# Performance work log

Measured on AMD Instinct MI355X. Metric: run time of the kernel, lower is better.

The kernel has to match this reference:

```python
import jax, jax.numpy as jnp
import numpy as np

B, S, M, K, V, E, NQ, C = 1024, 512, 64, 64, 128, 64, 10000, 4


def setup_inputs() -> dict:
    key = jax.random.key(0)
    ks = jax.random.split(key, 12)
    sc = 0.05  # small init so attention logits / predictions stay sane
    return {
        "q_ids": jax.random.randint(ks[0], (B, S), 0, NQ),
        "responses": jax.random.randint(ks[1], (B, S), 0, C),
        "q_table": jax.random.normal(ks[2], (NQ + 1, E), jnp.float32),
        "key_embeds": jax.random.normal(ks[3], (M, K), jnp.float32) * sc,
        "alpha_mean": jnp.zeros((M,), jnp.float32),
        "alpha_log_var": jnp.full((M,), np.log(0.3), jnp.float32),
        "beta_base": jnp.zeros((M,), jnp.float32),
        "beta_offsets": jnp.full((M, C - 1), 0.5, jnp.float32),
        "theta_mean0": jnp.zeros((M, V), jnp.float32),
        "theta_log_var0": jnp.zeros((M, V), jnp.float32),
        "q2k_w": jax.random.normal(ks[4], (E, K), jnp.float32) * sc,
        "q2k_b": jnp.zeros((K,), jnp.float32),
        "qa_w": jax.random.normal(ks[5], (2, E), jnp.float32) * sc,
        "qa_b": jnp.zeros((E,), jnp.float32),
        "qae_w": jax.random.normal(ks[6], (E, V), jnp.float32) * sc,
        "qae_b": jnp.zeros((V,), jnp.float32),
        "pred_w": jax.random.normal(ks[7], (V, 1), jnp.float32) * sc,
        "pred_b": jnp.zeros((1,), jnp.float32),
        "alpha_noise": jax.random.normal(ks[8], (S, M), jnp.float32),
        "beta_noise": jax.random.normal(ks[9], (S, M), jnp.float32),
    }


def reference(q_ids, responses, q_table, key_embeds, alpha_mean, alpha_log_var,
              beta_base, beta_offsets, theta_mean0, theta_log_var0,
              q2k_w, q2k_b, qa_w, qa_b, qae_w, qae_b, pred_w, pred_b,
              alpha_noise, beta_noise):
    # ---- question embeddings and DKVMN queries ----
    q_emb = q_table[q_ids]                                   # [B,S,E]
    query = q_emb @ q2k_w + q2k_b                            # [B,S,K]
    embed_sim = jnp.einsum('bsk,mk->bsm', query, key_embeds) # [B,S,M]

    # ---- per-slot IRT parameter sampling (vectorized over all 64 slots) ----
    alpha = jnp.exp(alpha_mean[None] + alpha_noise * jnp.exp(0.5 * alpha_log_var)[None])  # [S,M]
    base = beta_base[None] + beta_noise * 0.1                # [S,M]
    offs = jax.nn.softplus(beta_offsets)                     # [M,C-1]
    # beta[j] = base + sum_{k<j} offsets[k]  (ordered cumulative thresholds)
    cum = jnp.concatenate([jnp.zeros((M, 1), offs.dtype),
                           jnp.cumsum(offs, axis=1)[:, :C - 2]], axis=1)  # [M,C-1]
    beta_mean = base + cum.mean(axis=1)[None]                # [S,M]
    diff_sim = jnp.exp(-0.5 * beta_mean ** 2)                # [S,M]

    logits = embed_sim + 0.3 * alpha[None] + 0.2 * diff_sim[None]
    attn = jax.nn.softmax(logits, axis=-1)                   # [B,S,M]

    # ---- response evidence ----
    r_norm = responses.astype(jnp.float32) / (C - 1)         # [B,S]
    p = jnp.clip(r_norm, 0.01, 0.99)
    ability_ev = jnp.log(p) - jnp.log1p(-p)                  # logit, [B,S]
    ev_prec = 0.5 + jnp.abs(r_norm - 0.5) * 2.0              # [B,S]
    qa_in = jnp.stack([q_ids.astype(jnp.float32) / NQ, r_norm], axis=-1)  # [B,S,2]
    ev_embed = (qa_in @ qa_w + qa_b) @ qae_w + qae_b         # [B,S,V]

    # ---- sequential read / Bayesian write over memory state ----
    def step(carry, xs):
        th_m, th_lv = carry                                  # [M,V] each
        a, ee, ae, pr = xs                                   # [B,M],[B,V],[B],[B]
        # Bayesian read: attention-weighted belief mean
        cm = a @ th_m                                        # [B,V]
        pred = (cm @ pred_w + pred_b)[:, 0]                  # [B]
        # Bayesian write (torch does this under no_grad)
        a_norm = a / (a.sum(0) + 1e-8)                       # [B,M]
        comb = (ee + ae[:, None]) * 0.5                      # [B,V]
        agg_ev = jnp.einsum('bv,bm->mv', comb, a * a_norm)   # [M,V]
        agg_pr = a_norm.T @ pr                               # [M]
        w = a.mean(0)                                        # [M] update weight per slot
        prior_pr = jnp.exp(-th_lv)
        post_pr = prior_pr + (agg_pr * w)[:, None]
        post_m = (prior_pr * th_m + (agg_pr * w)[:, None] * agg_ev) / post_pr
        return (post_m, -jnp.log(post_pr)), pred

    xs = (attn.transpose(1, 0, 2), ev_embed.transpose(1, 0, 2),
          ability_ev.T, ev_prec.T)
    _, preds = jax.lax.scan(step, (theta_mean0, theta_log_var0), xs)
    return preds.T  # [B,S] predicted ability per (student, timestep)
```

## Files before the change

kernel.cpp:

```cpp
#include <hip/hip_runtime.h>


#define WS_EQ     0
#define WS_EB     640064
#define WS_PACK   672832
#define WS_PAT    1197120
#define WS_W1     1393728
#define WS_RDEN   1426496
#define WS_CONST  1950784
#define WS_P0     1950800
#define WS_Z0     1950864

__device__ __forceinline__ float wred_sum(float x) {
    x += __shfl_xor(x, 1);
    x += __shfl_xor(x, 2);
    x += __shfl_xor(x, 4);
    x += __shfl_xor(x, 8);
    x += __shfl_xor(x, 16);
    x += __shfl_xor(x, 32);
    return x;
}

__device__ __forceinline__ float softplusf(float x) {
    return fmaxf(x, 0.0f) + log1pf(__expf(-fabsf(x)));
}

__global__ __launch_bounds__(256) void k_prep(
    const int* __restrict__ q_ids, const int* __restrict__ responses,
    const float* __restrict__ q_table, const float* __restrict__ key_embeds,
    const float* __restrict__ q2k_w, const float* __restrict__ q2k_b,
    const float* __restrict__ alpha_mean, const float* __restrict__ alpha_log_var,
    const float* __restrict__ beta_base, const float* __restrict__ beta_offsets,
    const float* __restrict__ alpha_noise, const float* __restrict__ beta_noise,
    const float* __restrict__ qa_w, const float* __restrict__ qa_b,
    const float* __restrict__ qae_w, const float* __restrict__ qae_b,
    const float* __restrict__ pred_w,
    const float* __restrict__ th0, const float* __restrict__ lv0,
    float* __restrict__ ws)
{
    const int tid = threadIdx.x;
    const int bid = blockIdx.x;
    if (bid < 626) {
        __shared__ float sw[64 * 64];
        __shared__ float ske[64 * 65];
        for (int i = tid; i < 4096; i += 256) sw[i] = q2k_w[i];
        for (int i = tid; i < 4096; i += 256) ske[(i >> 6) * 65 + (i & 63)] = key_embeds[i];
        __syncthreads();
        const int wid = tid >> 6, lane = tid & 63;
        float* eq = ws + WS_EQ;
        for (int qq = 0; qq < 4; ++qq) {
            int q = bid * 16 + wid * 4 + qq;
            int qc = (q < 10001) ? q : 10000;
            float qe = q_table[qc * 64 + lane];
            float qk = q2k_b[lane];
            #pragma unroll
            for (int e = 0; e < 64; ++e)
                qk = fmaf(__shfl(qe, e), sw[e * 64 + lane], qk);
            float sim = 0.0f;
            #pragma unroll
            for (int k = 0; k < 64; ++k)
                sim = fmaf(__shfl(qk, k), ske[lane * 65 + k], sim);
            if (q < 10001) eq[q * 64 + lane] = __expf(sim);
        }
    } else if (bid < 658) {
        float* eb = ws + WS_EB;
        int base = (bid - 626) * 1024 + tid * 4;
        #pragma unroll
        for (int j = 0; j < 4; ++j) {
            int idx = base + j;
            int m = idx & 63;
            float sdev  = __expf(0.5f * alpha_log_var[m]);
            float alpha = __expf(fmaf(alpha_noise[idx], sdev, alpha_mean[m]));
            float bse   = fmaf(beta_noise[idx], 0.1f, beta_base[m]);
            float o0 = softplusf(beta_offsets[m * 3 + 0]);
            float o1 = softplusf(beta_offsets[m * 3 + 1]);
            float cmean = (o0 + (o0 + o1)) * (1.0f / 3.0f);
            float bm = bse + cmean;
            float diff = __expf(-0.5f * bm * bm);
            eb[idx] = __expf(fmaf(0.3f, alpha, 0.2f * diff));
        }
    } else if (bid == 658) {
        const int wid = tid >> 6, lane = tid & 63;
        if (wid == 0) {
            float qv = 0.0f;
            for (int v = 0; v < 128; ++v) qv = fmaf(qae_w[lane * 128 + v], pred_w[v], qv);
            float du  = wred_sum(qa_w[lane] * qv);
            float dw  = wred_sum(qa_w[64 + lane] * qv);
            float dc1 = wred_sum(qa_b[lane] * qv);
            float cb  = wred_sum(fmaf(qae_b[lane], pred_w[lane],
                                      qae_b[64 + lane] * pred_w[64 + lane]));
            float sp  = wred_sum(pred_w[lane] + pred_w[64 + lane]);
            if (lane == 0) {
                float* c = ws + WS_CONST;
                c[0] = du; c[1] = dw; c[2] = dc1 + cb; c[3] = sp;
            }
        } else if (wid == 1) {
            float z0 = 0.0f;
            for (int v = 0; v < 128; ++v) z0 = fmaf(th0[lane * 128 + v], pred_w[v], z0);
            ws[WS_Z0 + lane] = z0;
            ws[WS_P0 + lane] = __expf(-lv0[lane * 128]);
        }
    } else {
        int tb = bid - 659;
        int sb = tb & 7;
        int bb = tb >> 3;
        __shared__ int tile[64][65];
        #pragma unroll
        for (int j = 0; j < 16; ++j) {
            int row = (tid >> 6) * 16 + j;
            int col = tid & 63;
            int gi = (bb * 64 + row) * 512 + sb * 64 + col;
            tile[row][col] = q_ids[gi] | (responses[gi] << 16);
        }
        __syncthreads();
        int* packT = (int*)(ws + WS_PACK);
        #pragma unroll
        for (int j = 0; j < 16; ++j) {
            int row = (tid >> 6) * 16 + j;
            int col = tid & 63;
            packT[(sb * 64 + row) * 1024 + bb * 64 + col] = tile[col][row];
        }
    }
}

__global__ __launch_bounds__(512) void k_reduce(float* __restrict__ ws)
{
    const int bid = blockIdx.x;
    const int t = bid & 511, h = bid >> 9;
    const int tid = threadIdx.x;
    const int wid = tid >> 6, lane = tid & 63;
    const int r = lane >> 4, c = lane & 15;
    const float* eq = ws + WS_EQ;
    const int* packT = (const int*)(ws + WS_PACK);
    const float* cst = ws + WS_CONST;
    float* rden = ws + WS_RDEN;
    const float du = cst[0], dw = cst[1], dc = cst[2], sp = cst[3];

    float ae0, ae1, ae2, ae3;
    {
        float p;
        p = 0.01f;        ae0 = logf(p) - log1pf(-p);
        p = 0.33333334f;  ae1 = logf(p) - log1pf(-p);
        p = 0.6666667f;   ae2 = logf(p) - log1pf(-p);
        p = 0.99f;        ae3 = logf(p) - log1pf(-p);
    }

    const float4 ebv = *(const float4*)(ws + WS_EB + t * 64 + c * 4);
    const int bbase = h * 512 + wid * 64;

    float4 a1v = {0.f,0.f,0.f,0.f}, a2v = {0.f,0.f,0.f,0.f}, a3v = {0.f,0.f,0.f,0.f};
    #pragma unroll 4
    for (int i = 0; i < 16; ++i) {
        int b = bbase + i * 4 + r;
        int pk = packT[t * 1024 + b];
        int qid  = pk & 0xFFFF;
        int resp = pk >> 16;
        float rn = (float)resp * 0.33333334f;
        float ae = (resp == 0) ? ae0 : (resp == 1) ? ae1 : (resp == 2) ? ae2 : ae3;
        float pv = fmaf(fabsf(rn - 0.5f), 2.0f, 0.5f);
        float yv = fmaf(ae, sp, fmaf(rn, dw, fmaf((float)qid * 1e-4f, du, dc)));
        float4 eqv = *(const float4*)(eq + qid * 64 + c * 4);
        float4 e4;
        e4.x = eqv.x * ebv.x; e4.y = eqv.y * ebv.y;
        e4.z = eqv.z * ebv.z; e4.w = eqv.w * ebv.w;
        float s = (e4.x + e4.y) + (e4.z + e4.w);
        s += __shfl_xor(s, 1);
        s += __shfl_xor(s, 2);
        s += __shfl_xor(s, 4);
        s += __shfl_xor(s, 8);
        float rinv = __builtin_amdgcn_rcpf(s);
        if (c == 0) rden[b * 512 + t] = rinv;
        float4 a4;
        a4.x = e4.x * rinv; a4.y = e4.y * rinv; a4.z = e4.z * rinv; a4.w = e4.w * rinv;
        a1v.x += a4.x; a1v.y += a4.y; a1v.z += a4.z; a1v.w += a4.w;
        a2v.x = fmaf(a4.x, pv, a2v.x); a2v.y = fmaf(a4.y, pv, a2v.y);
        a2v.z = fmaf(a4.z, pv, a2v.z); a2v.w = fmaf(a4.w, pv, a2v.w);
        a3v.x = fmaf(a4.x * a4.x, yv, a3v.x); a3v.y = fmaf(a4.y * a4.y, yv, a3v.y);
        a3v.z = fmaf(a4.z * a4.z, yv, a3v.z); a3v.w = fmaf(a4.w * a4.w, yv, a3v.w);
    }
    #pragma unroll
    for (int d = 16; d <= 32; d <<= 1) {
        a1v.x += __shfl_xor(a1v.x, d); a1v.y += __shfl_xor(a1v.y, d);
        a1v.z += __shfl_xor(a1v.z, d); a1v.w += __shfl_xor(a1v.w, d);
        a2v.x += __shfl_xor(a2v.x, d); a2v.y += __shfl_xor(a2v.y, d);
        a2v.z += __shfl_xor(a2v.z, d); a2v.w += __shfl_xor(a2v.w, d);
        a3v.x += __shfl_xor(a3v.x, d); a3v.y += __shfl_xor(a3v.y, d);
        a3v.z += __shfl_xor(a3v.z, d); a3v.w += __shfl_xor(a3v.w, d);
    }

    __shared__ float red[8][3][64];
    if (lane < 16) {
        *(float4*)&red[wid][0][lane * 4] = a1v;
        *(float4*)&red[wid][1][lane * 4] = a2v;
        *(float4*)&red[wid][2][lane * 4] = a3v;
    }
    __syncthreads();
    if (wid == 0) {
        float A1 = 0.f, A2 = 0.f, A3 = 0.f;
        #pragma unroll
        for (int w = 0; w < 8; ++w) {
            A1 += red[w][0][lane]; A2 += red[w][1][lane]; A3 += red[w][2][lane];
        }
        float* pat = ws + WS_PAT;
        pat[(h * 64 + lane) * 512 + t]           = A1;
        pat[65536 + (h * 64 + lane) * 512 + t]   = A2;
        pat[131072 + (h * 64 + lane) * 512 + t]  = A3;
    }
}

__global__ __launch_bounds__(64) void k_scan(float* __restrict__ ws)
{
    const int m = blockIdx.x, lane = threadIdx.x;
    const float* pat = ws + WS_PAT;
    float A1[8], A2[8], A3[8];
    #pragma unroll
    for (int i = 0; i < 3; ++i) {
        const float* p0 = pat + i * 65536 + m * 512 + lane * 8;
        const float* p1 = p0 + 32768;
        float4 u0 = *(const float4*)p0, u1 = *(const float4*)(p0 + 4);
        float4 v0 = *(const float4*)p1, v1 = *(const float4*)(p1 + 4);
        float* A = (i == 0) ? A1 : (i == 1) ? A2 : A3;
        A[0] = u0.x + v0.x; A[1] = u0.y + v0.y; A[2] = u0.z + v0.z; A[3] = u0.w + v0.w;
        A[4] = u1.x + v1.x; A[5] = u1.y + v1.y; A[6] = u1.z + v1.z; A[7] = u1.w + v1.w;
    }
    float g[8], gz[8];
    #pragma unroll
    for (int j = 0; j < 8; ++j) {
        float denom = A1[j] + 1e-8f;
        float gg = (A2[j] / denom) * (A1[j] * (1.0f / 1024.0f));
        float zz = 0.5f * (A3[j] / denom);
        g[j] = gg; gz[j] = gg * zz;
    }
    float sg = 0.0f, sz = 0.0f;
    #pragma unroll
    for (int j = 0; j < 8; ++j) { sg += g[j]; sz += gz[j]; }
    #pragma unroll
    for (int d = 1; d < 64; d <<= 1) {
        float t1 = __shfl_up(sg, d);
        float t2 = __shfl_up(sz, d);
        if (lane >= d) { sg += t1; sz += t2; }
    }
    float eg = __shfl_up(sg, 1);
    float ez = __shfl_up(sz, 1);
    if (lane == 0) { eg = 0.0f; ez = 0.0f; }
    float P = ws[WS_P0 + m] + eg;
    float Z = ws[WS_Z0 + m] + ez;
    const float* eb = ws + WS_EB;
    float* w1 = ws + WS_W1;
    #pragma unroll
    for (int j = 0; j < 8; ++j) {
        int t = lane * 8 + j;
        w1[t * 64 + m] = (Z / P) * eb[t * 64 + m];
        Z += gz[j];
        P += g[j];
    }
}

__global__ __launch_bounds__(512) void k_pred(
    const int* __restrict__ q_ids, const float* __restrict__ pred_b,
    const float* __restrict__ ws, float* __restrict__ out)
{
    const int b = blockIdx.x;
    const int tid = threadIdx.x, wid = tid >> 6, lane = tid & 63;
    const int r = lane >> 4, c = lane & 15;
    const int t0 = wid * 64;
    const float* eq = ws + WS_EQ;
    const float* w1 = ws + WS_W1;
    const float* rden = ws + WS_RDEN;
    const float pb = pred_b[0];
    float keep = 0.0f;
    #pragma unroll 4
    for (int i = 0; i < 16; ++i) {
        int t = t0 + i * 4 + r;
        int qid = q_ids[b * 512 + t];
        float4 eqv = *(const float4*)(eq + qid * 64 + c * 4);
        float4 w1v = *(const float4*)(w1 + t * 64 + c * 4);
        float num = fmaf(eqv.w, w1v.w, fmaf(eqv.z, w1v.z, fmaf(eqv.y, w1v.y, eqv.x * w1v.x)));
        num += __shfl_xor(num, 1);
        num += __shfl_xor(num, 2);
        num += __shfl_xor(num, 4);
        num += __shfl_xor(num, 8);
        float v = __shfl(num, (lane & 3) * 16);
        if ((lane >> 2) == i) keep = v;
    }
    float rinv = rden[b * 512 + t0 + lane];
    out[b * 512 + t0 + lane] = fmaf(keep, rinv, pb);
}

extern "C" void kernel_launch(void* const* d_in, const int* in_sizes, int n_in,
                              void* d_out, int out_size, void* d_ws, size_t ws_size,
                              hipStream_t stream)
{
    (void)in_sizes; (void)n_in; (void)out_size; (void)ws_size;
    const int*   q_ids         = (const int*)d_in[0];
    const int*   responses     = (const int*)d_in[1];
    const float* q_table       = (const float*)d_in[2];
    const float* key_embeds    = (const float*)d_in[3];
    const float* alpha_mean    = (const float*)d_in[4];
    const float* alpha_log_var = (const float*)d_in[5];
    const float* beta_base     = (const float*)d_in[6];
    const float* beta_offsets  = (const float*)d_in[7];
    const float* th0           = (const float*)d_in[8];
    const float* lv0           = (const float*)d_in[9];
    const float* q2k_w         = (const float*)d_in[10];
    const float* q2k_b         = (const float*)d_in[11];
    const float* qa_w          = (const float*)d_in[12];
    const float* qa_b          = (const float*)d_in[13];
    const float* qae_w         = (const float*)d_in[14];
    const float* qae_b         = (const float*)d_in[15];
    const float* pred_w        = (const float*)d_in[16];
    const float* pred_bs       = (const float*)d_in[17];
    const float* alpha_noise   = (const float*)d_in[18];
    const float* beta_noise    = (const float*)d_in[19];
    float* ws  = (float*)d_ws;
    float* out = (float*)d_out;

    k_prep<<<dim3(787), dim3(256), 0, stream>>>(
        q_ids, responses, q_table, key_embeds, q2k_w, q2k_b,
        alpha_mean, alpha_log_var, beta_base, beta_offsets,
        alpha_noise, beta_noise, qa_w, qa_b, qae_w, qae_b,
        pred_w, th0, lv0, ws);
    k_reduce<<<dim3(1024), dim3(512), 0, stream>>>(ws);
    k_scan<<<dim3(64), dim3(64), 0, stream>>>(ws);
    k_pred<<<dim3(1024), dim3(512), 0, stream>>>(q_ids, pred_bs, ws, out);
}
```

Baseline: 172.7 us.

## Fold q2k_w and key_embeds into one projection matrix; LDS-based reduction in k_pred

Precomputes W2 = q2k_w·key_embedsᵀ and c0 = q2k_b·key_embedsᵀ in a new small kernel, so the question-similarity pass becomes a single 64x64 matvec per question instead of two chained ones with shuffles. The prep work is split into two launches, which adds one extra kernel launch. k_pred replaces the per-iteration shuffle reductions with per-thread partial sums written to shared memory and summed with vector LDS reads. The fp32 summation order changes slightly in both places.

```diff
diff --git a/kernel.cpp b/kernel.cpp
--- a/kernel.cpp
+++ b/kernel.cpp
@@ -10,6 +10,8 @@
 #define WS_CONST  1950784
 #define WS_P0     1950800
 #define WS_Z0     1950864
+#define WS_W2T    1950928
+#define WS_C0     1955024
 
 __device__ __forceinline__ float wred_sum(float x) {
     x += __shfl_xor(x, 1);
@@ -25,9 +27,9 @@
     return fmaxf(x, 0.0f) + log1pf(__expf(-fabsf(x)));
 }
 
-__global__ __launch_bounds__(256) void k_prep(
+__global__ __launch_bounds__(256) void k_pre0(
     const int* __restrict__ q_ids, const int* __restrict__ responses,
-    const float* __restrict__ q_table, const float* __restrict__ key_embeds,
+    const float* __restrict__ key_embeds,
     const float* __restrict__ q2k_w, const float* __restrict__ q2k_b,
     const float* __restrict__ alpha_mean, const float* __restrict__ alpha_log_var,
     const float* __restrict__ beta_base, const float* __restrict__ beta_offsets,
@@ -40,47 +42,26 @@
 {
     const int tid = threadIdx.x;
     const int bid = blockIdx.x;
-    if (bid < 626) {
-        __shared__ float sw[64 * 64];
-        __shared__ float ske[64 * 65];
-        for (int i = tid; i < 4096; i += 256) sw[i] = q2k_w[i];
-        for (int i = tid; i < 4096; i += 256) ske[(i >> 6) * 65 + (i & 63)] = key_embeds[i];
-        __syncthreads();
-        const int wid = tid >> 6, lane = tid & 63;
-        float* eq = ws + WS_EQ;
-        for (int qq = 0; qq < 4; ++qq) {
-            int q = bid * 16 + wid * 4 + qq;
-            int qc = (q < 10001) ? q : 10000;
-            float qe = q_table[qc * 64 + lane];
-            float qk = q2k_b[lane];
+    if (bid < 4) {
+        const int m = tid & 63;
+        const int esub = __builtin_amdgcn_readfirstlane(tid >> 6);
+        float kerow[64];
+        #pragma unroll
+        for (int j = 0; j < 16; ++j)
+            *(float4*)&kerow[j * 4] = *(const float4*)(key_embeds + m * 64 + j * 4);
+        float* w2t = ws + WS_W2T;
+        #pragma unroll
+        for (int jj = 0; jj < 4; ++jj) {
+            int e = bid * 16 + esub * 4 + jj;
+            const float* wrow = q2k_w + e * 64;
+            float acc = 0.0f;
             #pragma unroll
-            for (int e = 0; e < 64; ++e)
-                qk = fmaf(__shfl(qe, e), sw[e * 64 + lane], qk);
-            float sim = 0.0f;
-            #pragma unroll
-            for (int k = 0; k < 64; ++k)
-                sim = fmaf(__shfl(qk, k), ske[lane * 65 + k], sim);
-            if (q < 10001) eq[q * 64 + lane] = __expf(sim);
-        }
-    } else if (bid < 658) {
-        float* eb = ws + WS_EB;
-        int base = (bid - 626) * 1024 + tid * 4;
-        #pragma unroll
-        for (int j = 0; j < 4; ++j) {
-            int idx = base + j;
-            int m = idx & 63;
-            float sdev  = __expf(0.5f * alpha_log_var[m]);
-            float alpha = __expf(fmaf(alpha_noise[idx], sdev, alpha_mean[m]));
-            float bse   = fmaf(beta_noise[idx], 0.1f, beta_base[m]);
-            float o0 = softplusf(beta_offsets[m * 3 + 0]);
-            float o1 = softplusf(beta_offsets[m * 3 + 1]);
-            float cmean = (o0 + (o0 + o1)) * (1.0f / 3.0f);
-            float bm = bse + cmean;
-            float diff = __expf(-0.5f * bm * bm);
-            eb[idx] = __expf(fmaf(0.3f, alpha, 0.2f * diff));
-        }
-    } else if (bid == 658) {
-        const int wid = tid >> 6, lane = tid & 63;
+            for (int k = 0; k < 64; ++k) acc = fmaf(wrow[k], kerow[k], acc);
+            w2t[m * 64 + e] = acc;
+        }
+    } else if (bid == 4) {
+        const int wid = __builtin_amdgcn_readfirstlane(tid >> 6);
+        const int lane = tid & 63;
         if (wid == 0) {
             float qv = 0.0f;
             for (int v = 0; v < 128; ++v) qv = fmaf(qae_w[lane * 128 + v], pred_w[v], qv);
@@ -99,9 +80,31 @@
             for (int v = 0; v < 128; ++v) z0 = fmaf(th0[lane * 128 + v], pred_w[v], z0);
             ws[WS_Z0 + lane] = z0;
             ws[WS_P0 + lane] = __expf(-lv0[lane * 128]);
+        } else if (wid == 2) {
+            float acc = 0.0f;
+            #pragma unroll
+            for (int k = 0; k < 64; ++k) acc = fmaf(q2k_b[k], key_embeds[lane * 64 + k], acc);
+            ws[WS_C0 + lane] = acc;
+        }
+    } else if (bid < 37) {
+        float* eb = ws + WS_EB;
+        int base = (bid - 5) * 1024 + tid * 4;
+        #pragma unroll
+        for (int j = 0; j < 4; ++j) {
+            int idx = base + j;
+            int m = idx & 63;
+            float sdev  = __expf(0.5f * alpha_log_var[m]);
+            float alpha = __expf(fmaf(alpha_noise[idx], sdev, alpha_mean[m]));
+            float bse   = fmaf(beta_noise[idx], 0.1f, beta_base[m]);
+            float o0 = softplusf(beta_offsets[m * 3 + 0]);
+            float o1 = softplusf(beta_offsets[m * 3 + 1]);
+            float cmean = (o0 + (o0 + o1)) * (1.0f / 3.0f);
+            float bm = bse + cmean;
+            float diff = __expf(-0.5f * bm * bm);
+            eb[idx] = __expf(fmaf(0.3f, alpha, 0.2f * diff));
         }
     } else {
-        int tb = bid - 659;
+        int tb = bid - 37;
         int sb = tb & 7;
         int bb = tb >> 3;
         __shared__ int tile[64][65];
@@ -120,6 +123,33 @@
             int col = tid & 63;
             packT[(sb * 64 + row) * 1024 + bb * 64 + col] = tile[col][row];
         }
+    }
+}
+
+__global__ __launch_bounds__(256) void k_prep(
+    const float* __restrict__ q_table, float* __restrict__ ws)
+{
+    const int tid = threadIdx.x;
+    const int bid = blockIdx.x;
+    const int wid = __builtin_amdgcn_readfirstlane(tid >> 6);
+    const int lane = tid & 63;
+    float w2row[64];
+    const float* w2t = ws + WS_W2T + lane * 64;
+    #pragma unroll
+    for (int j = 0; j < 16; ++j)
+        *(float4*)&w2row[j * 4] = *(const float4*)(w2t + j * 4);
+    const float c0 = ws[WS_C0 + lane];
+    float* eq = ws + WS_EQ;
+    #pragma unroll
+    for (int qq = 0; qq < 4; ++qq) {
+        int q = bid * 16 + wid * 4 + qq;
+        int qc = (q < 10001) ? q : 10000;
+        const float* qrow = q_table + qc * 64;
+        float sim = c0;
+        #pragma unroll
+        for (int e = 0; e < 64; ++e)
+            sim = fmaf(qrow[e], w2row[e], sim);
+        if (q < 10001) eq[q * 64 + lane] = __expf(sim);
     }
 }
 
@@ -268,23 +298,28 @@
     const float* w1 = ws + WS_W1;
     const float* rden = ws + WS_RDEN;
     const float pb = pred_b[0];
-    float keep = 0.0f;
+    float acc[16];
     #pragma unroll 4
     for (int i = 0; i < 16; ++i) {
         int t = t0 + i * 4 + r;
         int qid = q_ids[b * 512 + t];
         float4 eqv = *(const float4*)(eq + qid * 64 + c * 4);
         float4 w1v = *(const float4*)(w1 + t * 64 + c * 4);
-        float num = fmaf(eqv.w, w1v.w, fmaf(eqv.z, w1v.z, fmaf(eqv.y, w1v.y, eqv.x * w1v.x)));
-        num += __shfl_xor(num, 1);
-        num += __shfl_xor(num, 2);
-        num += __shfl_xor(num, 4);
-        num += __shfl_xor(num, 8);
-        float v = __shfl(num, (lane & 3) * 16);
-        if ((lane >> 2) == i) keep = v;
-    }
+        acc[i] = fmaf(eqv.w, w1v.w, fmaf(eqv.z, w1v.z, fmaf(eqv.y, w1v.y, eqv.x * w1v.x)));
+    }
+    __shared__ float part[8 * 64 * 20];
+    float* p = part + wid * 64 * 20;
+    #pragma unroll
+    for (int i = 0; i < 16; ++i)
+        p[(i * 4 + r) * 20 + c] = acc[i];
+    float4 s0 = *(const float4*)(p + lane * 20);
+    float4 s1 = *(const float4*)(p + lane * 20 + 4);
+    float4 s2 = *(const float4*)(p + lane * 20 + 8);
+    float4 s3 = *(const float4*)(p + lane * 20 + 12);
+    float num = ((s0.x + s0.y) + (s0.z + s0.w)) + ((s1.x + s1.y) + (s1.z + s1.w))
+              + ((s2.x + s2.y) + (s2.z + s2.w)) + ((s3.x + s3.y) + (s3.z + s3.w));
     float rinv = rden[b * 512 + t0 + lane];
-    out[b * 512 + t0 + lane] = fmaf(keep, rinv, pb);
+    out[b * 512 + t0 + lane] = fmaf(num, rinv, pb);
 }
 
 extern "C" void kernel_launch(void* const* d_in, const int* in_sizes, int n_in,
@@ -315,11 +350,12 @@
     float* ws  = (float*)d_ws;
     float* out = (float*)d_out;
 
-    k_prep<<<dim3(787), dim3(256), 0, stream>>>(
-        q_ids, responses, q_table, key_embeds, q2k_w, q2k_b,
+    k_pre0<<<dim3(165), dim3(256), 0, stream>>>(
+        q_ids, responses, key_embeds, q2k_w, q2k_b,
         alpha_mean, alpha_log_var, beta_base, beta_offsets,
         alpha_noise, beta_noise, qa_w, qa_b, qae_w, qae_b,
         pred_w, th0, lv0, ws);
+    k_prep<<<dim3(626), dim3(256), 0, stream>>>(q_table, ws);
     k_reduce<<<dim3(1024), dim3(512), 0, stream>>>(ws);
     k_scan<<<dim3(64), dim3(64), 0, stream>>>(ws);
     k_pred<<<dim3(1024), dim3(512), 0, stream>>>(q_ids, pred_bs, ws, out);
```

After: 152.6 us (median of 2 runs). -11.6%, faster.
